# Performance work log

Hardware: AMD Instinct MI355X
Metric: run time of the kernel (lower is better)

The kernel has to match this reference:

```python
import jax, jax.numpy as jnp
import numpy as np

N = 50000   # nodes
E = 400000  # edges per relation
R = 3       # relations
IN, HID, OUT, H = 256, 64, 64, 4
NEG_SLOPE = 0.2


def setup_inputs() -> dict:
    key = jax.random.key(0)
    ks = jax.random.split(key, 16)
    w = lambda k, shape, s: jax.random.normal(k, shape, jnp.float32) * s
    sW = 1.0 / np.sqrt(IN)  # ~xavier scale (all fan-ins are 256)
    return {
        "x":   w(ks[0], (N, IN), 1.0),
        "src": jax.random.randint(ks[1], (R, E), 0, N, jnp.int32),
        "dst": jax.random.randint(ks[2], (R, E), 0, N, jnp.int32),
        "W0":  w(ks[3], (R, IN, H * HID), sW),
        "al0": w(ks[4], (R, H, HID), 0.1),
        "ar0": w(ks[5], (R, H, HID), 0.1),
        "b0":  jnp.zeros((R, H * HID), jnp.float32),
        "W1":  w(ks[6], (R, H * HID, H * HID), sW),
        "al1": w(ks[7], (R, H, HID), 0.1),
        "ar1": w(ks[8], (R, H, HID), 0.1),
        "b1":  jnp.zeros((R, H * HID), jnp.float32),
        "W2":  w(ks[9], (R, H * HID, H * OUT), sW),
        "al2": w(ks[10], (R, H, OUT), 0.1),
        "ar2": w(ks[11], (R, H, OUT), 0.1),
        "b2":  jnp.zeros((R, H * OUT), jnp.float32),
    }


def gat_conv(h, src, dst, W, al, ar, b):
    """One DGL-style GATConv with elu activation. h: (N, F_in)."""
    heads, d = al.shape
    feat = (h @ W).reshape(-1, heads, d)               # (N, H, D)
    el = jnp.einsum('nhd,hd->nh', feat, al)            # (N, H)
    er = jnp.einsum('nhd,hd->nh', feat, ar)
    e = jax.nn.leaky_relu(el[src] + er[dst], NEG_SLOPE)  # (E, H)
    # segment softmax over incoming edges of each dst node
    emax = jax.ops.segment_max(e, dst, num_segments=N)
    ex = jnp.exp(e - emax[dst])
    denom = jax.ops.segment_sum(ex, dst, num_segments=N)
    alpha = ex / jnp.maximum(denom[dst], 1e-9)         # (E, H)
    msg = feat[src] * alpha[:, :, None]                # (E, H, D)
    out = jax.ops.segment_sum(msg, dst, num_segments=N)  # (N, H, D)
    out = out + b.reshape(heads, d)
    return jax.nn.elu(out)


def _rgat(x, src, dst, params):
    h = x
    for li, (W, al, ar, b) in enumerate(params):
        outs = [gat_conv(h, src[r], dst[r], W[r], al[r], ar[r], b[r]) for r in range(R)]
        o = sum(outs) / R                              # cross-relation mean, (N, H, D)
        h = o.mean(1) if li == 2 else o.reshape(N, -1)
    return h


def reference(x, src, dst, W0, al0, ar0, b0, W1, al1, ar1, b1, W2, al2, ar2, b2):
    params = [(W0, al0, ar0, b0), (W1, al1, ar1, b1), (W2, al2, ar2, b2)]
    return _rgat(x, src, dst, params)
```

## Files before the change

kernel.cpp:

```cpp
#include <hip/hip_runtime.h>
#include <hip/hip_bf16.h>

#define N_NODES 50000
#define N_EDGES 400000
#define N_REL   3
#define NEG_SLOPE 0.2f
#define RP_STRIDE 50016
#define SCAN_BLOCKS 49
#define M_TILES 391
#define MG_PER_XCD 49
#define M_PAD 50048
#define MAXDEG 48

typedef __bf16 bf16x8 __attribute__((ext_vector_type(8)));
typedef float  f32x4  __attribute__((ext_vector_type(4)));

static __device__ __forceinline__ float bf2f(unsigned short u) {
  return __uint_as_float(((unsigned)u) << 16);
}
static __device__ __forceinline__ unsigned short f2bf(float f) {
  union { float f; unsigned u; } x; x.f = f;
  unsigned r = x.u + 0x7FFFu + ((x.u >> 16) & 1u);
  return (unsigned short)(r >> 16);
}
static __device__ __forceinline__ void gld16(const void* g, unsigned short* lds) {
  __builtin_amdgcn_global_load_lds(
      (const __attribute__((address_space(1))) unsigned int*)g,
      (__attribute__((address_space(3))) unsigned int*)lds, 16, 0, 0);
}


__global__ void count_kernel(const int* __restrict__ dst, int* __restrict__ cnt, int total) {
  int i = blockIdx.x * 256 + threadIdx.x;
  if (i < total) {
    int r = i / N_EDGES;
    atomicAdd(&cnt[r * N_NODES + dst[i]], 1);
  }
}

__global__ void block_reduce_kernel(const int* __restrict__ cnt, int* __restrict__ psum) {
  __shared__ int s[256];
  int r = blockIdx.x / SCAN_BLOCKS, b = blockIdx.x % SCAN_BLOCKS;
  int node = b * 1024 + threadIdx.x * 4;
  int sum = 0;
  if (node + 3 < N_NODES) {
    int4 v = *(const int4*)&cnt[r * N_NODES + node];
    sum = v.x + v.y + v.z + v.w;
  } else {
    for (int j = 0; j < 4; j++)
      if (node + j < N_NODES) sum += cnt[r * N_NODES + node + j];
  }
  s[threadIdx.x] = sum;
  __syncthreads();
  for (int o = 128; o > 0; o >>= 1) {
    if (threadIdx.x < o) s[threadIdx.x] += s[threadIdx.x + o];
    __syncthreads();
  }
  if (threadIdx.x == 0) psum[r * SCAN_BLOCKS + b] = s[0];
}

__global__ void psum_scan_kernel(int* __restrict__ psum, int* __restrict__ row_ptr) {
  int r = blockIdx.x, t = threadIdx.x;
  int v = (t < SCAN_BLOCKS) ? psum[r * SCAN_BLOCKS + t] : 0;
  int incl = v;
#pragma unroll
  for (int o = 1; o < 64; o <<= 1) {
    int u = __shfl_up(incl, o);
    if (t >= o) incl += u;
  }
  if (t < SCAN_BLOCKS) psum[r * SCAN_BLOCKS + t] = incl - v;
  if (t == SCAN_BLOCKS - 1) row_ptr[r * RP_STRIDE + N_NODES] = incl;
}

__global__ void scan_write_kernel(const int* __restrict__ cnt, const int* __restrict__ psum,
                                  int* __restrict__ row_ptr, int* __restrict__ cursor) {
  __shared__ int s[256];
  int r = blockIdx.x / SCAN_BLOCKS, b = blockIdx.x % SCAN_BLOCKS;
  int tid = threadIdx.x;
  int node = b * 1024 + tid * 4;
  int c[4] = {0, 0, 0, 0};
  if (node + 3 < N_NODES) {
    int4 v = *(const int4*)&cnt[r * N_NODES + node];
    c[0] = v.x; c[1] = v.y; c[2] = v.z; c[3] = v.w;
  } else {
    for (int j = 0; j < 4; j++)
      if (node + j < N_NODES) c[j] = cnt[r * N_NODES + node + j];
  }
  int tsum = c[0] + c[1] + c[2] + c[3];
  s[tid] = tsum;
  __syncthreads();
  for (int o = 1; o < 256; o <<= 1) {
    int v = (tid >= o) ? s[tid - o] : 0;
    __syncthreads();
    s[tid] += v;
    __syncthreads();
  }
  int run = s[tid] - tsum + psum[r * SCAN_BLOCKS + b];
  if (node + 3 < N_NODES) {
    int4 rp = make_int4(run, run + c[0], run + c[0] + c[1], run + c[0] + c[1] + c[2]);
    *(int4*)&row_ptr[r * RP_STRIDE + node] = rp;
    *(int4*)&cursor[r * N_NODES + node] = rp;
  } else {
    for (int j = 0; j < 4; j++) {
      if (node + j < N_NODES) {
        row_ptr[r * RP_STRIDE + node + j] = run;
        cursor[r * N_NODES + node + j] = run;
      }
      run += c[j];
    }
  }
}

__global__ void scatter_kernel(const int* __restrict__ src, const int* __restrict__ dst,
                               int* __restrict__ cursor, int* __restrict__ col, int total) {
  int i = blockIdx.x * 256 + threadIdx.x;
  if (i < total) {
    int r = i / N_EDGES;
    int d = dst[i];
    int pos = atomicAdd(&cursor[r * N_NODES + d], 1);
    col[r * N_EDGES + pos] = src[i];
  }
}


__global__ void xsplit_kernel(const float* __restrict__ x, unsigned short* __restrict__ xh) {
  int i = blockIdx.x * 256 + threadIdx.x;
  int row = i >> 6;
  float4 v = make_float4(0.f, 0.f, 0.f, 0.f);
  if (row < N_NODES) v = ((const float4*)x)[i];
  ushort4 h;
  h.x = f2bf(v.x); h.y = f2bf(v.y); h.z = f2bf(v.z); h.w = f2bf(v.w);
  ((ushort4*)xh)[i] = h;
}


__global__ void wsplit_kernel(const float* __restrict__ W0, const float* __restrict__ W1,
                              const float* __restrict__ W2,
                              unsigned short* __restrict__ Whi, unsigned short* __restrict__ Wlo) {
  __shared__ float tile[32][33];
  int mat = blockIdx.x >> 6;
  int t = blockIdx.x & 63;
  int k0 = (t >> 3) * 32, n0 = (t & 7) * 32;
  const float* W = (mat < 3 ? W0 : (mat < 6 ? W1 : W2)) + (size_t)(mat % 3) * 65536;
  int row = threadIdx.x >> 3;
  int c4 = threadIdx.x & 7;
  float4 v = *(const float4*)&W[(k0 + row) * 256 + n0 + c4 * 4];
  tile[c4 * 4 + 0][row] = v.x;
  tile[c4 * 4 + 1][row] = v.y;
  tile[c4 * 4 + 2][row] = v.z;
  tile[c4 * 4 + 3][row] = v.w;
  __syncthreads();
  int nl = threadIdx.x >> 3;
  int kq = threadIdx.x & 7;
  ushort4 h, l;
  float a0 = tile[nl][kq * 4 + 0], a1 = tile[nl][kq * 4 + 1];
  float a2 = tile[nl][kq * 4 + 2], a3 = tile[nl][kq * 4 + 3];
  h.x = f2bf(a0); l.x = f2bf(a0 - bf2f(h.x));
  h.y = f2bf(a1); l.y = f2bf(a1 - bf2f(h.y));
  h.z = f2bf(a2); l.z = f2bf(a2 - bf2f(h.z));
  h.w = f2bf(a3); l.w = f2bf(a3 - bf2f(h.w));
  size_t o = (size_t)mat * 65536 + (n0 + nl) * 256 + k0 + kq * 4;
  *(ushort4*)&Whi[o] = h;
  *(ushort4*)&Wlo[o] = l;
}


#define LDS_S 32
#define LDT  136

__global__ __launch_bounds__(256, 3) void gemm_mfma_kernel(
    const unsigned short* __restrict__ Ah,
    const unsigned short* __restrict__ Bhi, const unsigned short* __restrict__ Blo,
    const float* __restrict__ alf, const float* __restrict__ arf,
    unsigned short* __restrict__ Cb, float* __restrict__ el, float* __restrict__ er, int M) {
  __shared__ __align__(16) unsigned short lds[128 * LDT];
  unsigned short* As_h = lds;
  unsigned short* Bs_h = lds + 128 * LDS_S;
  unsigned short* Bs_l = lds + 2 * 128 * LDS_S;

  const int wid = blockIdx.x;
  const int xcd = wid & 7, local = wid >> 3;
  const int m_t = (local / 6) * 8 + xcd;
  if (m_t >= M_TILES) return;
  const int n_t = local % 6;
  const int m0 = m_t * 128, n0 = n_t * 128;

  const int tid = threadIdx.x;
  const int wave = tid >> 6, lane = tid & 63;
  const int quad = lane >> 4, l16 = lane & 15;
  const int wr = wave & 1, wc = wave >> 1;

  f32x4 acc[4][4];
#pragma unroll
  for (int i = 0; i < 4; i++)
#pragma unroll
    for (int j = 0; j < 4; j++) acc[i][j] = (f32x4){0.f, 0.f, 0.f, 0.f};

  for (int kb = 0; kb < 8; kb++) {
    int k0 = kb * 32;
#pragma unroll
    for (int i = 0; i < 2; i++) {
      int ch = wave * 2 + i;
      int c = ch * 64 + lane;
      int row = c >> 2, k16 = c & 3;
      size_t gA = ((size_t)(m0 + row) * 256 + k0) * 2 + (size_t)k16 * 16;
      size_t gB = ((size_t)(n0 + row) * 256 + k0) * 2 + (size_t)k16 * 16;
      gld16((const char*)Ah + gA, &As_h[ch * 512]);
      gld16((const char*)Bhi + gB, &Bs_h[ch * 512]);
      gld16((const char*)Blo + gB, &Bs_l[ch * 512]);
    }
    __syncthreads();

    bf16x8 ah[4], bh[4], bl[4];
#pragma unroll
    for (int t = 0; t < 4; t++) {
      int arow = (wr * 64 + t * 16 + l16) * LDS_S + quad * 8;
      int brow = (wc * 64 + t * 16 + l16) * LDS_S + quad * 8;
      ah[t] = *(const bf16x8*)&As_h[arow];
      bh[t] = *(const bf16x8*)&Bs_h[brow];
      bl[t] = *(const bf16x8*)&Bs_l[brow];
    }
#pragma unroll
    for (int mi = 0; mi < 4; mi++)
#pragma unroll
      for (int ni = 0; ni < 4; ni++) {
        acc[mi][ni] = __builtin_amdgcn_mfma_f32_16x16x32_bf16(ah[mi], bl[ni], acc[mi][ni], 0, 0, 0);
        acc[mi][ni] = __builtin_amdgcn_mfma_f32_16x16x32_bf16(ah[mi], bh[ni], acc[mi][ni], 0, 0, 0);
      }
    __syncthreads();
  }

  const int hw = n_t * 2 + wc;
  const int rel = hw >> 2, hh = hw & 3;
  float alw[4], arw[4];
#pragma unroll
  for (int ni = 0; ni < 4; ni++) {
    int gc = n0 + wc * 64 + ni * 16 + l16;
    alw[ni] = alf[gc]; arw[ni] = arf[gc];
  }
  float pel[4][4], per_[4][4];
#pragma unroll
  for (int mi = 0; mi < 4; mi++)
#pragma unroll
    for (int r = 0; r < 4; r++) {
      float se = 0.f, sr = 0.f;
#pragma unroll
      for (int ni = 0; ni < 4; ni++) {
        se += acc[mi][ni][r] * alw[ni];
        sr += acc[mi][ni][r] * arw[ni];
      }
      pel[mi][r] = se; per_[mi][r] = sr;
    }
#pragma unroll
  for (int off = 1; off < 16; off <<= 1)
#pragma unroll
    for (int mi = 0; mi < 4; mi++)
#pragma unroll
      for (int r = 0; r < 4; r++) {
        pel[mi][r] += __shfl_xor(pel[mi][r], off);
        per_[mi][r] += __shfl_xor(per_[mi][r], off);
      }
  if (l16 == 0) {
#pragma unroll
    for (int mi = 0; mi < 4; mi++)
#pragma unroll
      for (int r = 0; r < 4; r++) {
        int gm = m0 + wr * 64 + mi * 16 + quad * 4 + r;
        if (gm < M) {
          size_t o = ((size_t)rel * N_NODES + gm) * 4 + hh;
          el[o] = pel[mi][r];
          er[o] = per_[mi][r];
        }
      }
  }

#pragma unroll
  for (int mi = 0; mi < 4; mi++) {
    int row = wr * 64 + mi * 16 + quad * 4;
#pragma unroll
    for (int ni = 0; ni < 4; ni++) {
      int c = wc * 64 + ni * 16 + l16;
#pragma unroll
      for (int r = 0; r < 4; r++)
        lds[(row + r) * LDT + c] = f2bf(acc[mi][ni][r]);
    }
  }
  __syncthreads();
#pragma unroll
  for (int it = 0; it < 8; it++) {
    int chunk = tid + 256 * it;
    int row = chunk >> 4, c8 = (chunk & 15) * 8;
    int gm = m0 + row;
    if (gm < M)
      *(uint4*)&Cb[(size_t)gm * 768 + n0 + c8] = *(const uint4*)&lds[row * LDT + c8];
  }
}


__global__ void agg_kernel(const unsigned short* __restrict__ featb,
                           const float* __restrict__ el, const float* __restrict__ er,
                           const int* __restrict__ row_ptr, const int* __restrict__ col,
                           const float* __restrict__ bias,
                           unsigned short* __restrict__ hH, float* __restrict__ outF,
                           int final_layer) {
  __shared__ float salpha[4][N_REL][MAXDEG * 4];
  __shared__ int   sidx[4][N_REL][MAXDEG];
  int w = threadIdx.x >> 6;
  int n = blockIdx.x * 4 + w;
  int L = threadIdx.x & 63;
  if (n >= N_NODES) return;
  const int hsel = L >> 4;

  int s0r[N_REL], s1r[N_REL];
  float invsel[N_REL];
  float4 ernr[N_REL];

  int sv[N_REL];
  bool val[N_REL], fastp[N_REL];
#pragma unroll
  for (int r = 0; r < N_REL; r++) {
    int s0 = row_ptr[r * RP_STRIDE + n], s1 = row_ptr[r * RP_STRIDE + n + 1];
    s0r[r] = s0; s1r[r] = s1;
    int deg = s1 - s0;
    fastp[r] = (deg <= 64);
    int i = s0 + L;
    val[r] = fastp[r] && (i < s1);
    sv[r] = 0;
    if (val[r]) sv[r] = col[(size_t)r * N_EDGES + i];
    ernr[r] = ((const float4*)er)[(size_t)r * N_NODES + n];
  }
  float4 ev[N_REL];
#pragma unroll
  for (int r = 0; r < N_REL; r++) {
    ev[r] = make_float4(0.f, 0.f, 0.f, 0.f);
    if (val[r]) ev[r] = ((const float4*)el)[(size_t)r * N_NODES + sv[r]];
  }
#pragma unroll
  for (int r = 0; r < N_REL; r++) {
    float4 ern = ernr[r];
    float p0 = 0.f, p1 = 0.f, p2 = 0.f, p3 = 0.f;
    if (val[r]) {
      float e0 = ev[r].x + ern.x; e0 = e0 > 0.f ? e0 : NEG_SLOPE * e0;
      float e1 = ev[r].y + ern.y; e1 = e1 > 0.f ? e1 : NEG_SLOPE * e1;
      float e2 = ev[r].z + ern.z; e2 = e2 > 0.f ? e2 : NEG_SLOPE * e2;
      float e3 = ev[r].w + ern.w; e3 = e3 > 0.f ? e3 : NEG_SLOPE * e3;
      p0 = __expf(e0); p1 = __expf(e1); p2 = __expf(e2); p3 = __expf(e3);
    }
    float d0 = p0, d1 = p1, d2 = p2, d3 = p3;
    if (!fastp[r]) {
      int s0 = s0r[r], s1 = s1r[r];
      const int* cp = col + (size_t)r * N_EDGES;
      for (int base = s0; base < s1; base += 64) {
        int i = base + L;
        if (i < s1) {
          int s = cp[i];
          float4 els = ((const float4*)el)[(size_t)r * N_NODES + s];
          float e0 = els.x + ern.x; e0 = e0 > 0.f ? e0 : NEG_SLOPE * e0;
          float e1 = els.y + ern.y; e1 = e1 > 0.f ? e1 : NEG_SLOPE * e1;
          float e2 = els.z + ern.z; e2 = e2 > 0.f ? e2 : NEG_SLOPE * e2;
          float e3 = els.w + ern.w; e3 = e3 > 0.f ? e3 : NEG_SLOPE * e3;
          d0 += __expf(e0); d1 += __expf(e1); d2 += __expf(e2); d3 += __expf(e3);
        }
      }
    }
#pragma unroll
    for (int o = 1; o < 64; o <<= 1) {
      d0 += __shfl_xor(d0, o); d1 += __shfl_xor(d1, o);
      d2 += __shfl_xor(d2, o); d3 += __shfl_xor(d3, o);
    }
    float i0 = 1.0f / fmaxf(d0, 1e-30f), i1 = 1.0f / fmaxf(d1, 1e-30f);
    float i2 = 1.0f / fmaxf(d2, 1e-30f), i3 = 1.0f / fmaxf(d3, 1e-30f);
    invsel[r] = (hsel == 0) ? i0 : (hsel == 1) ? i1 : (hsel == 2) ? i2 : i3;
    int deg = s1r[r] - s0r[r];
    if (val[r] && deg <= MAXDEG) {
      *(float4*)&salpha[w][r][L * 4] = make_float4(p0 * i0, p1 * i1, p2 * i2, p3 * i3);
      sidx[w][r][L] = sv[r];
    }
  }

  const float third = 1.0f / 3.0f;
  const int roffL = 4 * L;
  float os0 = 0.f, os1 = 0.f, os2 = 0.f, os3 = 0.f;
#pragma unroll
  for (int r = 0; r < N_REL; r++) {
    int s0 = s0r[r], s1 = s1r[r], deg = s1 - s0;
    const int roff = r * 256 + roffL;
    float a0 = 0.f, a1 = 0.f, a2 = 0.f, a3 = 0.f;
    if (deg <= MAXDEG) {
      const float* ap = &salpha[w][r][0];
      const int* ip = &sidx[w][r][0];
      int i = 0;
      for (; i + 8 <= deg; i += 8) {
        int s_[8];
#pragma unroll
        for (int j = 0; j < 8; j++) s_[j] = ip[i + j];
        ushort4 f_[8];
#pragma unroll
        for (int j = 0; j < 8; j++) {
          size_t ro = (size_t)(unsigned)__builtin_amdgcn_readfirstlane(s_[j]) * 768;
          f_[j] = *(const ushort4*)&featb[ro + roff];
        }
        float w_[8];
#pragma unroll
        for (int j = 0; j < 8; j++) w_[j] = ap[(i + j) * 4 + hsel];
#pragma unroll
        for (int j = 0; j < 8; j++) {
          a0 += w_[j] * bf2f(f_[j].x);
          a1 += w_[j] * bf2f(f_[j].y);
          a2 += w_[j] * bf2f(f_[j].z);
          a3 += w_[j] * bf2f(f_[j].w);
        }
      }
      for (; i + 4 <= deg; i += 4) {
        int s_[4];
#pragma unroll
        for (int j = 0; j < 4; j++) s_[j] = ip[i + j];
        ushort4 f_[4];
#pragma unroll
        for (int j = 0; j < 4; j++) {
          size_t ro = (size_t)(unsigned)__builtin_amdgcn_readfirstlane(s_[j]) * 768;
          f_[j] = *(const ushort4*)&featb[ro + roff];
        }
        float w_[4];
#pragma unroll
        for (int j = 0; j < 4; j++) w_[j] = ap[(i + j) * 4 + hsel];
#pragma unroll
        for (int j = 0; j < 4; j++) {
          a0 += w_[j] * bf2f(f_[j].x);
          a1 += w_[j] * bf2f(f_[j].y);
          a2 += w_[j] * bf2f(f_[j].z);
          a3 += w_[j] * bf2f(f_[j].w);
        }
      }
      for (; i < deg; i++) {
        int sA = ip[i];
        size_t ro = (size_t)(unsigned)__builtin_amdgcn_readfirstlane(sA) * 768;
        ushort4 fA = *(const ushort4*)&featb[ro + roff];
        float wA = ap[i * 4 + hsel];
        a0 += wA * bf2f(fA.x); a1 += wA * bf2f(fA.y);
        a2 += wA * bf2f(fA.z); a3 += wA * bf2f(fA.w);
      }
      float4 bv = *(const float4*)&bias[r * 256 + roffL];
      float o0 = a0 + bv.x, o1 = a1 + bv.y, o2 = a2 + bv.z, o3 = a3 + bv.w;
      o0 = o0 > 0.f ? o0 : __expf(o0) - 1.0f;
      o1 = o1 > 0.f ? o1 : __expf(o1) - 1.0f;
      o2 = o2 > 0.f ? o2 : __expf(o2) - 1.0f;
      o3 = o3 > 0.f ? o3 : __expf(o3) - 1.0f;
      os0 += o0 * third; os1 += o1 * third; os2 += o2 * third; os3 += o3 * third;
    } else {
      float4 ern = ernr[r];
      float ernh = (hsel == 0) ? ern.x : (hsel == 1) ? ern.y : (hsel == 2) ? ern.z : ern.w;
      const int* cp = col + (size_t)r * N_EDGES;
      for (int i = s0; i < s1; i++) {
        int s = cp[i];
        float4 els = ((const float4*)el)[(size_t)r * N_NODES + s];
        float elh = (hsel == 0) ? els.x : (hsel == 1) ? els.y : (hsel == 2) ? els.z : els.w;
        float e = elh + ernh; e = e > 0.f ? e : NEG_SLOPE * e;
        float pw = __expf(e);
        ushort4 fA = *(const ushort4*)&featb[(size_t)s * 768 + roff];
        a0 += pw * bf2f(fA.x); a1 += pw * bf2f(fA.y);
        a2 += pw * bf2f(fA.z); a3 += pw * bf2f(fA.w);
      }
      float inv = invsel[r];
      float4 bv = *(const float4*)&bias[r * 256 + roffL];
      float o0 = a0 * inv + bv.x, o1 = a1 * inv + bv.y;
      float o2 = a2 * inv + bv.z, o3 = a3 * inv + bv.w;
      o0 = o0 > 0.f ? o0 : __expf(o0) - 1.0f;
      o1 = o1 > 0.f ? o1 : __expf(o1) - 1.0f;
      o2 = o2 > 0.f ? o2 : __expf(o2) - 1.0f;
      o3 = o3 > 0.f ? o3 : __expf(o3) - 1.0f;
      os0 += o0 * third; os1 += o1 * third; os2 += o2 * third; os3 += o3 * third;
    }
  }
  if (final_layer) {
#pragma unroll
    for (int o = 16; o <= 32; o <<= 1) {
      os0 += __shfl_xor(os0, o); os1 += __shfl_xor(os1, o);
      os2 += __shfl_xor(os2, o); os3 += __shfl_xor(os3, o);
    }
    if (L < 16)
      *(float4*)&outF[(size_t)n * 64 + L * 4] =
          make_float4(0.25f * os0, 0.25f * os1, 0.25f * os2, 0.25f * os3);
  } else {
    ushort4 h;
    h.x = f2bf(os0); h.y = f2bf(os1); h.z = f2bf(os2); h.w = f2bf(os3);
    *(ushort4*)&hH[(size_t)n * 256 + 4 * L] = h;
  }
}


extern "C" void kernel_launch(void* const* d_in, const int* in_sizes, int n_in,
                              void* d_out, int out_size, void* d_ws, size_t ws_size,
                              hipStream_t stream) {
  (void)in_sizes; (void)n_in; (void)out_size; (void)ws_size;
  const float* x = (const float*)d_in[0];
  const int* src = (const int*)d_in[1];
  const int* dst = (const int*)d_in[2];
  const float* Wl[3]  = {(const float*)d_in[3], (const float*)d_in[7], (const float*)d_in[11]};
  const float* alL[3] = {(const float*)d_in[4], (const float*)d_in[8], (const float*)d_in[12]};
  const float* arL[3] = {(const float*)d_in[5], (const float*)d_in[9], (const float*)d_in[13]};
  const float* bL[3]  = {(const float*)d_in[6], (const float*)d_in[10], (const float*)d_in[14]};

  char* p = (char*)d_ws;
  auto alloc = [&](size_t bytes) {
    char* q = p;
    p += (bytes + 255) & ~size_t(255);
    return q;
  };
  unsigned short* xh = (unsigned short*)alloc((size_t)M_PAD * 256 * 2);
  unsigned short* hH = (unsigned short*)alloc((size_t)M_PAD * 256 * 2);
  unsigned short* featb = (unsigned short*)alloc((size_t)N_NODES * 768 * 2);
  float* el      = (float*)alloc((size_t)N_REL * N_NODES * 4 * 4);
  float* er      = (float*)alloc((size_t)N_REL * N_NODES * 4 * 4);
  int*   cnt     = (int*)alloc((size_t)N_REL * N_NODES * 4);
  int*   cursor  = (int*)alloc((size_t)N_REL * N_NODES * 4);
  int*   row_ptr = (int*)alloc((size_t)N_REL * RP_STRIDE * 4 + 64);
  int*   col     = (int*)alloc((size_t)N_REL * N_EDGES * 4);
  int*   psum    = (int*)alloc((size_t)N_REL * SCAN_BLOCKS * 4);
  unsigned short* Whi = (unsigned short*)alloc((size_t)9 * 65536 * 2);
  unsigned short* Wlo = (unsigned short*)alloc((size_t)9 * 65536 * 2);

  hipMemsetAsync(cnt, 0, (size_t)N_REL * N_NODES * 4, stream);
  const int totalE = N_REL * N_EDGES;
  count_kernel<<<(totalE + 255) / 256, 256, 0, stream>>>(dst, cnt, totalE);
  block_reduce_kernel<<<N_REL * SCAN_BLOCKS, 256, 0, stream>>>(cnt, psum);
  psum_scan_kernel<<<N_REL, 64, 0, stream>>>(psum, row_ptr);
  scan_write_kernel<<<N_REL * SCAN_BLOCKS, 256, 0, stream>>>(cnt, psum, row_ptr, cursor);
  scatter_kernel<<<(totalE + 255) / 256, 256, 0, stream>>>(src, dst, cursor, col, totalE);
  wsplit_kernel<<<9 * 64, 256, 0, stream>>>(Wl[0], Wl[1], Wl[2], Whi, Wlo);
  xsplit_kernel<<<M_PAD * 64 / 256, 256, 0, stream>>>(x, xh);

  const int nodeBlocks = (N_NODES + 3) / 4;
  const int gemmBlocks = MG_PER_XCD * 6 * 8;
  for (int l = 0; l < 3; l++) {
    const unsigned short* Ahp = (l == 0) ? xh : hH;
    gemm_mfma_kernel<<<gemmBlocks, 256, 0, stream>>>(
        Ahp, Whi + (size_t)l * 3 * 65536, Wlo + (size_t)l * 3 * 65536,
        alL[l], arL[l], featb, el, er, N_NODES);
    agg_kernel<<<nodeBlocks, 256, 0, stream>>>(
        featb, el, er, row_ptr, col, bL[l], hH, (float*)d_out, l == 2);
  }
}
```

Before: 763.4 us.

## Double-buffer GEMM LDS stages and XOR-swizzle tile layout

The MFMA GEMM's shared-memory tile is split into two buffers so the next k-block's global-to-LDS loads are issued before the current block's MFMAs run, overlapping memory latency with compute. The 16-byte chunk index is XOR-swizzled by row on both the load and read sides to cut LDS bank conflicts on the fragment reads. LDS use changes from 128*136 to 2*3*4096 shorts, which may affect occupancy and the epilogue if it reuses the old larger LDS region. The trailing barrier inside the loop is not visible here, so buffer reuse safety relies on the unchanged loop tail.

Measured after the change: 756.3 us. About the same (-0.9%).

```diff
diff --git a/kernel.cpp b/kernel.cpp
--- a/kernel.cpp
+++ b/kernel.cpp
@@ -167,16 +167,15 @@
 
 #define LDS_S 32
 #define LDT  136
+#define PLANE 4096
+#define BUFSZ (3 * PLANE)
 
 __global__ __launch_bounds__(256, 3) void gemm_mfma_kernel(
     const unsigned short* __restrict__ Ah,
     const unsigned short* __restrict__ Bhi, const unsigned short* __restrict__ Blo,
     const float* __restrict__ alf, const float* __restrict__ arf,
     unsigned short* __restrict__ Cb, float* __restrict__ el, float* __restrict__ er, int M) {
-  __shared__ __align__(16) unsigned short lds[128 * LDT];
-  unsigned short* As_h = lds;
-  unsigned short* Bs_h = lds + 128 * LDS_S;
-  unsigned short* Bs_l = lds + 2 * 128 * LDS_S;
+  __shared__ __align__(16) unsigned short lds[2 * BUFSZ];
 
   const int wid = blockIdx.x;
   const int xcd = wid & 7, local = wid >> 3;
@@ -196,29 +195,41 @@
 #pragma unroll
     for (int j = 0; j < 4; j++) acc[i][j] = (f32x4){0.f, 0.f, 0.f, 0.f};
 
-  for (int kb = 0; kb < 8; kb++) {
-    int k0 = kb * 32;
+  auto stage = [&](int kb, int b) {
+    unsigned short* As = lds + b * BUFSZ;
 #pragma unroll
     for (int i = 0; i < 2; i++) {
       int ch = wave * 2 + i;
       int c = ch * 64 + lane;
       int row = c >> 2, k16 = c & 3;
-      size_t gA = ((size_t)(m0 + row) * 256 + k0) * 2 + (size_t)k16 * 16;
-      size_t gB = ((size_t)(n0 + row) * 256 + k0) * 2 + (size_t)k16 * 16;
-      gld16((const char*)Ah + gA, &As_h[ch * 512]);
-      gld16((const char*)Bhi + gB, &Bs_h[ch * 512]);
-      gld16((const char*)Blo + gB, &Bs_l[ch * 512]);
-    }
-    __syncthreads();
-
+      int k16s = k16 ^ ((row >> 1) & 3);
+      size_t gA = ((size_t)(m0 + row) * 256 + kb * 32) * 2 + (size_t)k16s * 16;
+      size_t gB = ((size_t)(n0 + row) * 256 + kb * 32) * 2 + (size_t)k16s * 16;
+      gld16((const char*)Ah + gA, &As[ch * 512]);
+      gld16((const char*)Bhi + gB, &As[PLANE + ch * 512]);
+      gld16((const char*)Blo + gB, &As[2 * PLANE + ch * 512]);
+    }
+  };
+
+  stage(0, 0);
+  __syncthreads();
+  for (int kb = 0; kb < 8; kb++) {
+    const int b = kb & 1;
+    if (kb < 7) stage(kb + 1, b ^ 1);
+
+    const unsigned short* As = lds + b * BUFSZ;
+    const unsigned short* Bh = As + PLANE;
+    const unsigned short* Bl = As + 2 * PLANE;
     bf16x8 ah[4], bh[4], bl[4];
 #pragma unroll
     for (int t = 0; t < 4; t++) {
-      int arow = (wr * 64 + t * 16 + l16) * LDS_S + quad * 8;
-      int brow = (wc * 64 + t * 16 + l16) * LDS_S + quad * 8;
-      ah[t] = *(const bf16x8*)&As_h[arow];
-      bh[t] = *(const bf16x8*)&Bs_h[brow];
-      bl[t] = *(const bf16x8*)&Bs_l[brow];
+      int ar = wr * 64 + t * 16 + l16;
+      int br = wc * 64 + t * 16 + l16;
+      int ac = quad ^ ((ar >> 1) & 3);
+      int bc = quad ^ ((br >> 1) & 3);
+      ah[t] = *(const bf16x8*)&As[ar * LDS_S + ac * 8];
+      bh[t] = *(const bf16x8*)&Bh[br * LDS_S + bc * 8];
+      bl[t] = *(const bf16x8*)&Bl[br * LDS_S + bc * 8];
     }
 #pragma unroll
     for (int mi = 0; mi < 4; mi++)
```
